# Kernel tuning notes

Hardware: AMD Instinct MI355X
Metric: run time of the kernel (lower is better)

## Reference

```python
import jax, jax.numpy as jnp
import numpy as np

N = 10000      # nodes
E = 160000     # edges (before self-loops)
H = 8          # heads
D_IN, D_H1, D_H2 = 165, 128, 1    # per-head channels of gat1 / gat2
HID = H * D_H1                    # 1024


def batchnorm(x, gamma, beta, eps=1e-5):
    # training-mode BatchNorm1d: biased batch statistics over the node axis
    mu = x.mean(0)
    var = x.var(0)
    return (x - mu) * jax.lax.rsqrt(var + eps) * gamma + beta


def gatv2(x, src, dst, Wl, bl, Wr, br, att, bias, heads, out_ch, concat, n_nodes):
    # PyG GATv2Conv: lin_l on source, lin_r on target; e = att . LeakyReLU(xl_j + xr_i)
    xl = (x @ Wl + bl).reshape(n_nodes, heads, out_ch)   # source transform
    xr = (x @ Wr + br).reshape(n_nodes, heads, out_ch)   # target transform
    e = jax.nn.leaky_relu(xl[src] + xr[dst], 0.2)        # [E,H,C]
    logits = jnp.einsum('ehc,hc->eh', e, att)            # [E,H]
    # segment softmax over incoming edges of each destination node
    m = jax.lax.stop_gradient(jax.ops.segment_max(logits, dst, num_segments=n_nodes))
    a = jnp.exp(logits - m[dst])
    s = jax.ops.segment_sum(a, dst, num_segments=n_nodes)
    alpha = a / (s[dst] + 1e-16)                          # [E,H]
    out = jax.ops.segment_sum(xl[src] * alpha[..., None], dst, num_segments=n_nodes)
    out = out.reshape(n_nodes, heads * out_ch) if concat else out.mean(1)
    return out + bias


def setup_inputs() -> dict:
    key = jax.random.key(0)
    ks = jax.random.split(key, 12)
    g = lambda k, shape, fan_in: jax.random.normal(k, shape, jnp.float32) * (1.0 / np.sqrt(fan_in))
    return {
        'x': jax.random.normal(ks[0], (N, D_IN), jnp.float32),
        'gamma1': jnp.ones((D_IN,), jnp.float32),
        'beta1': jnp.zeros((D_IN,), jnp.float32),
        'Wl1': g(ks[1], (D_IN, HID), D_IN),
        'bl1': jnp.zeros((HID,), jnp.float32),
        'Wr1': g(ks[2], (D_IN, HID), D_IN),
        'br1': jnp.zeros((HID,), jnp.float32),
        'att1': g(ks[3], (H, D_H1), D_H1),
        'bias1': jnp.zeros((HID,), jnp.float32),
        'gamma2': jnp.ones((HID,), jnp.float32),
        'beta2': jnp.zeros((HID,), jnp.float32),
        'Wl2': g(ks[4], (HID, H * D_H2), HID),
        'bl2': jnp.zeros((H * D_H2,), jnp.float32),
        'Wr2': g(ks[5], (HID, H * D_H2), HID),
        'br2': jnp.zeros((H * D_H2,), jnp.float32),
        'att2': g(ks[6], (H, D_H2), D_H2),
        'bias2': jnp.zeros((D_H2,), jnp.float32),
        'edge_index': jax.random.randint(ks[7], (2, E), 0, N, jnp.int64 if jax.config.jax_enable_x64 else jnp.int32),
    }


def reference(x, gamma1, beta1, Wl1, bl1, Wr1, br1, att1, bias1,
              gamma2, beta2, Wl2, bl2, Wr2, br2, att2, bias2, edge_index):
    loops = jnp.arange(N, dtype=edge_index.dtype)
    src = jnp.concatenate([edge_index[0], loops])   # add_self_loops=True (PyG default)
    dst = jnp.concatenate([edge_index[1], loops])
    h = batchnorm(x, gamma1, beta1)
    h = gatv2(h, src, dst, Wl1, bl1, Wr1, br1, att1, bias1, H, D_H1, True, N)
    h = batchnorm(h, gamma2, beta2)
    h = jax.nn.leaky_relu(h, 0.01)                  # F.leaky_relu default slope
    out = gatv2(h, src, dst, Wl2, bl2, Wr2, br2, att2, bias2, H, D_H2, False, N)
    return out
```

## Files before the change

### kernel.cpp

```cpp
#include <hip/hip_runtime.h>

#define NN   10000
#define E0   160000
#define ET   170000
#define DIN  165
#define KP   192
#define HID  1024
#define NH   8
#define BP   200
#define K2P  1032


typedef __bf16 bf16x8 __attribute__((ext_vector_type(8)));
typedef float  f32x4  __attribute__((ext_vector_type(4)));

__device__ __forceinline__ float bf2f(unsigned short u) {
    unsigned int i = ((unsigned int)u) << 16;
    return __builtin_bit_cast(float, i);
}
__device__ __forceinline__ unsigned short f2bf(float f) {
    unsigned int i = __builtin_bit_cast(unsigned int, f);
    i += 0x7fffu + ((i >> 16) & 1u);
    return (unsigned short)(i >> 16);
}
__device__ __forceinline__ float fin(float x) {
    return fminf(fmaxf(x, -1e30f), 1e30f);
}
__device__ __forceinline__ int clampi(int s) {
    return min(max(s, 0), NN - 1);
}
__device__ __forceinline__ void unpack8(uint4 u, float* f) {
    f[0]=bf2f((unsigned short)(u.x)); f[1]=bf2f((unsigned short)(u.x>>16));
    f[2]=bf2f((unsigned short)(u.y)); f[3]=bf2f((unsigned short)(u.y>>16));
    f[4]=bf2f((unsigned short)(u.z)); f[5]=bf2f((unsigned short)(u.z>>16));
    f[6]=bf2f((unsigned short)(u.w)); f[7]=bf2f((unsigned short)(u.w>>16));
}

__global__ __launch_bounds__(256) void debug_fill(float* __restrict__ out, float val) {
    int i = blockIdx.x * 256 + threadIdx.x;
    if (i < NN) out[i] = val;
}

__global__ __launch_bounds__(256) void bn1_stats(const float* __restrict__ x,
                                                 float* __restrict__ colsum, float* __restrict__ colsq) {
    int r0 = blockIdx.x * 125;
    int c = threadIdx.x;
    if (c >= DIN) return;
    float acc = 0.f, sq = 0.f;
    for (int r = r0; r < r0 + 125; ++r) {
        float v = x[(size_t)r * DIN + c];
        acc += v; sq += v * v;
    }
    atomicAdd(&colsum[c], acc);
    atomicAdd(&colsq[c], sq);
}

__global__ __launch_bounds__(256) void bn1_apply(const float* __restrict__ x,
                                                 const float* __restrict__ colsum, const float* __restrict__ colsq,
                                                 const float* __restrict__ gamma, const float* __restrict__ beta,
                                                 unsigned short* __restrict__ hn) {
    int idx = blockIdx.x * 256 + threadIdx.x;
    if (idx >= NN * KP) return;
    int r = idx / KP, c = idx - r * KP;
    float v = 0.f;
    if (c < DIN) {
        float mu  = colsum[c] * (1.f / NN);
        float var = fmaxf(colsq[c] * (1.f / NN) - mu * mu, 0.f);
        float a = gamma[c] * rsqrtf(var + 1e-5f);
        float b = beta[c] - mu * a;
        v = fin(x[(size_t)r * DIN + c] * a + b);
    }
    hn[idx] = f2bf(v);
}

__global__ __launch_bounds__(256) void w1_transpose(const float* __restrict__ wl,
                                                    const float* __restrict__ wr,
                                                    unsigned short* __restrict__ wlt,
                                                    unsigned short* __restrict__ wrt) {
    const float* src    = blockIdx.z ? wr  : wl;
    unsigned short* dst = blockIdx.z ? wrt : wlt;
    __shared__ float ts[32][65];
    const int k0 = blockIdx.x * 32;
    const int n0 = blockIdx.y * 64;
    const int tid = threadIdx.x;
    for (int idx = tid; idx < 32 * 64; idx += 256) {
        int k = idx >> 6, n = idx & 63;
        ts[k][n] = (k0 + k < DIN) ? src[(size_t)(k0 + k) * HID + n0 + n] : 0.f;
    }
    __syncthreads();
    for (int idx = tid; idx < 64 * 32; idx += 256) {
        int n = idx >> 5, k = idx & 31;
        dst[(size_t)(n0 + n) * KP + k0 + k] = f2bf(ts[k][n]);
    }
}

__global__ __launch_bounds__(256) void gemm1_kernel(
    const unsigned short* __restrict__ hn,
    const unsigned short* __restrict__ wlt,
    const unsigned short* __restrict__ wrt,
    const float* __restrict__ bl,
    const float* __restrict__ br,
    unsigned short* __restrict__ xl,
    unsigned short* __restrict__ xr) {
    const unsigned short* wt = blockIdx.z ? wrt : wlt;
    const float* bias        = blockIdx.z ? br  : bl;
    unsigned short* xout     = blockIdx.z ? xr  : xl;

    __shared__ unsigned short bs[64 * BP];
    const int tid  = threadIdx.x;
    const int lane = tid & 63;
    const int wave = tid >> 6;
    const int col  = lane & 15;
    const int q    = lane >> 4;
    const int n0   = blockIdx.y * 64;

    for (int idx = tid; idx < 64 * 48; idx += 256) {
        int r = idx / 48, c = idx - r * 48;
        uint2 v = *(const uint2*)(wt + (size_t)(n0 + r) * KP + c * 4);
        *(uint2*)&bs[r * BP + c * 4] = v;
    }
    __syncthreads();

    const int mbase = blockIdx.x * 128 + wave * 32;
    const int am0 = mbase + col;
    const int am1 = am0 + 16;
    const bool aok0 = (am0 < NN), aok1 = (am1 < NN);

    f32x4 acc[2][4];
    #pragma unroll
    for (int m = 0; m < 2; ++m)
        for (int nt = 0; nt < 4; ++nt)
            for (int r = 0; r < 4; ++r) acc[m][nt][r] = 0.f;

    #pragma unroll
    for (int kt = 0; kt < 6; ++kt) {
        const int kk = kt * 32 + q * 8;
        uint4 a0u = make_uint4(0u,0u,0u,0u), a1u = make_uint4(0u,0u,0u,0u);
        if (aok0) a0u = *(const uint4*)(hn + (size_t)am0 * KP + kk);
        if (aok1) a1u = *(const uint4*)(hn + (size_t)am1 * KP + kk);
        bf16x8 a0 = __builtin_bit_cast(bf16x8, a0u);
        bf16x8 a1 = __builtin_bit_cast(bf16x8, a1u);
        #pragma unroll
        for (int nt = 0; nt < 4; ++nt) {
            bf16x8 bf = __builtin_bit_cast(bf16x8, *(const uint4*)&bs[(nt * 16 + col) * BP + kk]);
            acc[0][nt] = __builtin_amdgcn_mfma_f32_16x16x32_bf16(a0, bf, acc[0][nt], 0, 0, 0);
            acc[1][nt] = __builtin_amdgcn_mfma_f32_16x16x32_bf16(a1, bf, acc[1][nt], 0, 0, 0);
        }
    }

    #pragma unroll
    for (int nt = 0; nt < 4; ++nt) {
        const int nc = n0 + nt * 16 + col;
        const float bv = bias[nc];
        #pragma unroll
        for (int m = 0; m < 2; ++m) {
            #pragma unroll
            for (int r = 0; r < 4; ++r) {
                const int row = mbase + m * 16 + q * 4 + r;
                if (row < NN)
                    xout[(size_t)row * HID + nc] = f2bf(fin(acc[m][nt][r] + bv));
            }
        }
    }
}

__global__ __launch_bounds__(256) void edge_hist(const int* __restrict__ ei, int* __restrict__ deg) {
    int e = blockIdx.x * 256 + threadIdx.x;
    if (e >= ET) return;
    int d = (e < E0) ? ei[E0 + e] : (e - E0);
    atomicAdd(&deg[clampi(d)], 1);
}

__global__ __launch_bounds__(1024) void scan_kernel(const int* __restrict__ deg,
                                                    int* __restrict__ offs, int* __restrict__ cur) {
    __shared__ int wsum[16];
    const int tid = threadIdx.x;
    const int base = tid * 10;
    int loc[10];
    int run = 0;
    #pragma unroll
    for (int j = 0; j < 10; ++j) {
        int idx = base + j;
        int v = (idx < NN) ? deg[idx] : 0;
        loc[j] = run;
        run += v;
    }
    const int lane = tid & 63;
    const int w = tid >> 6;
    int inc = run;
    #pragma unroll
    for (int s = 1; s < 64; s <<= 1) {
        int t = __shfl_up(inc, s);
        if (lane >= s) inc += t;
    }
    if (lane == 63) wsum[w] = inc;
    __syncthreads();
    int woff = 0;
    #pragma unroll
    for (int k = 0; k < 16; ++k) woff += (k < w) ? wsum[k] : 0;
    const int toff = woff + inc - run;
    #pragma unroll
    for (int j = 0; j < 10; ++j) {
        int idx = base + j;
        if (idx < NN) { int e = toff + loc[j]; offs[idx] = e; cur[idx] = e; }
    }
    if (tid == 1023) offs[NN] = woff + inc;
}

__global__ __launch_bounds__(256) void edge_scatter(const int* __restrict__ ei,
                                                    int* __restrict__ cur, int* __restrict__ ssrc) {
    int e = blockIdx.x * 256 + threadIdx.x;
    if (e >= ET) return;
    int s, d;
    if (e < E0) { s = ei[e]; d = ei[E0 + e]; }
    else        { s = e - E0; d = e - E0; }
    int pos = atomicAdd(&cur[clampi(d)], 1);
    if (pos >= 0 && pos < ET) ssrc[pos] = clampi(s);
}

__global__ __launch_bounds__(256) void gat1_node(
    const unsigned short* __restrict__ xl1, const unsigned short* xr1,
    const float* __restrict__ att1, const float* __restrict__ bias1,
    const int* __restrict__ offs, const int* __restrict__ ssrc,
    unsigned short* agg) {
    const int lane = threadIdx.x & 63;
    const int wave = threadIdx.x >> 6;
    const int i = blockIdx.x * 4 + wave;
    const int e0 = offs[i];
    const int e1 = max(offs[i + 1], e0);

    float xr_r[16], att_r[16];
    {
        const uint4* xp = (const uint4*)(xr1 + (size_t)i * HID + lane * 16);
        uint4 u0 = xp[0], u1 = xp[1];
        unpack8(u0, xr_r); unpack8(u1, xr_r + 8);
        const float4* ap = (const float4*)(att1 + lane * 16);
        float4 a0 = ap[0], a1 = ap[1], a2 = ap[2], a3 = ap[3];
        att_r[0]=a0.x; att_r[1]=a0.y; att_r[2]=a0.z; att_r[3]=a0.w;
        att_r[4]=a1.x; att_r[5]=a1.y; att_r[6]=a1.z; att_r[7]=a1.w;
        att_r[8]=a2.x; att_r[9]=a2.y; att_r[10]=a2.z; att_r[11]=a2.w;
        att_r[12]=a3.x; att_r[13]=a3.y; att_r[14]=a3.z; att_r[15]=a3.w;
    }

    float o[16];
    #pragma unroll
    for (int j = 0; j < 16; ++j) o[j] = 0.f;
    float s = 0.f;

    int e = e0;
    for (; e + 1 < e1; e += 2) {
        const int s0i = clampi(ssrc[e]);
        const int s1i = clampi(ssrc[e + 1]);
        const uint4* xp0 = (const uint4*)(xl1 + (size_t)s0i * HID + lane * 16);
        const uint4* xp1 = (const uint4*)(xl1 + (size_t)s1i * HID + lane * 16);
        uint4 a0 = xp0[0], a1 = xp0[1], b0 = xp1[0], b1 = xp1[1];
        float xv0[16], xv1[16];
        unpack8(a0, xv0); unpack8(a1, xv0 + 8);
        unpack8(b0, xv1); unpack8(b1, xv1 + 8);
        float p0 = 0.f, p1 = 0.f;
        #pragma unroll
        for (int j = 0; j < 16; ++j) {
            float v0 = xv0[j] + xr_r[j];
            float v1 = xv1[j] + xr_r[j];
            v0 = fmaxf(v0, 0.2f * v0);
            v1 = fmaxf(v1, 0.2f * v1);
            p0 = fmaf(att_r[j], v0, p0);
            p1 = fmaf(att_r[j], v1, p1);
        }
        p0 += __shfl_xor(p0, 1); p0 += __shfl_xor(p0, 2); p0 += __shfl_xor(p0, 4);
        p1 += __shfl_xor(p1, 1); p1 += __shfl_xor(p1, 2); p1 += __shfl_xor(p1, 4);
        const float aa0 = __expf(fminf(fin(p0), 50.f));
        const float aa1 = __expf(fminf(fin(p1), 50.f));
        s += aa0 + aa1;
        #pragma unroll
        for (int j = 0; j < 16; ++j) o[j] = fmaf(aa0, xv0[j], fmaf(aa1, xv1[j], o[j]));
    }
    if (e < e1) {
        const int sidx = clampi(ssrc[e]);
        const uint4* xp = (const uint4*)(xl1 + (size_t)sidx * HID + lane * 16);
        uint4 u0 = xp[0], u1 = xp[1];
        float xv[16];
        unpack8(u0, xv); unpack8(u1, xv + 8);
        float p = 0.f;
        #pragma unroll
        for (int j = 0; j < 16; ++j) {
            float v = xv[j] + xr_r[j];
            v = fmaxf(v, 0.2f * v);
            p = fmaf(att_r[j], v, p);
        }
        p += __shfl_xor(p, 1); p += __shfl_xor(p, 2); p += __shfl_xor(p, 4);
        const float a = __expf(fminf(fin(p), 50.f));
        s += a;
        #pragma unroll
        for (int j = 0; j < 16; ++j) o[j] = fmaf(a, xv[j], o[j]);
    }

    const float inv = 1.f / (s + 1e-16f);
    const float4* bp = (const float4*)(bias1 + lane * 16);
    float4 b0 = bp[0], b1 = bp[1], b2 = bp[2], b3 = bp[3];
    float bb[16] = {b0.x,b0.y,b0.z,b0.w, b1.x,b1.y,b1.z,b1.w,
                    b2.x,b2.y,b2.z,b2.w, b3.x,b3.y,b3.z,b3.w};
    unsigned short ov[16];
    #pragma unroll
    for (int j = 0; j < 16; ++j) ov[j] = f2bf(fin(o[j] * inv + bb[j]));
    uint4* op = (uint4*)(agg + (size_t)i * HID + lane * 16);
    op[0] = *(const uint4*)&ov[0];
    op[1] = *(const uint4*)&ov[8];
}

__global__ __launch_bounds__(256) void bn2_stats(const unsigned short* __restrict__ agg,
                                                 float* __restrict__ colsum, float* __restrict__ colsq) {
    int r0 = blockIdx.x * 125;
    int t = threadIdx.x;
    float s0=0,s1=0,s2=0,s3=0,q0=0,q1=0,q2=0,q3=0;
    for (int r = r0; r < r0 + 125; ++r) {
        const ushort4 u = *(const ushort4*)(agg + (size_t)r * HID + t * 4);
        float v0=bf2f(u.x), v1=bf2f(u.y), v2=bf2f(u.z), v3=bf2f(u.w);
        s0+=v0; q0+=v0*v0; s1+=v1; q1+=v1*v1;
        s2+=v2; q2+=v2*v2; s3+=v3; q3+=v3*v3;
    }
    atomicAdd(&colsum[t*4+0], s0); atomicAdd(&colsq[t*4+0], q0);
    atomicAdd(&colsum[t*4+1], s1); atomicAdd(&colsq[t*4+1], q1);
    atomicAdd(&colsum[t*4+2], s2); atomicAdd(&colsq[t*4+2], q2);
    atomicAdd(&colsum[t*4+3], s3); atomicAdd(&colsq[t*4+3], q3);
}

__global__ __launch_bounds__(256) void bn2_apply(unsigned short* __restrict__ agg,
                                                 const float* __restrict__ colsum, const float* __restrict__ colsq,
                                                 const float* __restrict__ gamma, const float* __restrict__ beta) {
    int idx = blockIdx.x * 256 + threadIdx.x;
    int base = idx * 4;
    int c = base & (HID - 1);
    ushort4 u = *(const ushort4*)(agg + base);
    float4 cs = *(const float4*)(colsum + c);
    float4 cq = *(const float4*)(colsq + c);
    float4 g  = *(const float4*)(gamma + c);
    float4 bt = *(const float4*)(beta + c);
    float mu0 = cs.x*(1.f/NN), mu1 = cs.y*(1.f/NN), mu2 = cs.z*(1.f/NN), mu3 = cs.w*(1.f/NN);
    float a0 = g.x * rsqrtf(fmaxf(cq.x*(1.f/NN)-mu0*mu0, 0.f) + 1e-5f);
    float a1 = g.y * rsqrtf(fmaxf(cq.y*(1.f/NN)-mu1*mu1, 0.f) + 1e-5f);
    float a2 = g.z * rsqrtf(fmaxf(cq.z*(1.f/NN)-mu2*mu2, 0.f) + 1e-5f);
    float a3 = g.w * rsqrtf(fmaxf(cq.w*(1.f/NN)-mu3*mu3, 0.f) + 1e-5f);
    float o0 = bf2f(u.x)*a0 + (bt.x - mu0*a0);
    float o1 = bf2f(u.y)*a1 + (bt.y - mu1*a1);
    float o2 = bf2f(u.z)*a2 + (bt.z - mu2*a2);
    float o3 = bf2f(u.w)*a3 + (bt.w - mu3*a3);
    o0 = fmaxf(o0, 0.01f * o0); o1 = fmaxf(o1, 0.01f * o1);
    o2 = fmaxf(o2, 0.01f * o2); o3 = fmaxf(o3, 0.01f * o3);
    ushort4 o; o.x = f2bf(fin(o0)); o.y = f2bf(fin(o1)); o.z = f2bf(fin(o2)); o.w = f2bf(fin(o3));
    *(ushort4*)(agg + base) = o;
}

__global__ __launch_bounds__(256) void gemm2_kernel(
    const unsigned short* __restrict__ h2,
    const float* __restrict__ wl2, const float* __restrict__ wr2,
    const float* __restrict__ bl2, const float* __restrict__ br2,
    float* __restrict__ xl2, float* __restrict__ xr2) {
    __shared__ unsigned short bs[16 * K2P];
    const int tid  = threadIdx.x;
    const int lane = tid & 63;
    const int wave = tid >> 6;
    const int col  = lane & 15;
    const int q    = lane >> 4;

    for (int idx = tid; idx < 16 * HID; idx += 256) {
        int n = idx >> 10, k = idx & (HID - 1);
        float v = (n < 8) ? wl2[k * 8 + n] : wr2[k * 8 + (n - 8)];
        bs[n * K2P + k] = f2bf(v);
    }
    __syncthreads();

    const int mtile = blockIdx.x * 4 + wave;
    if (mtile >= NN / 16) return;
    const int m0 = mtile * 16;
    const int am = m0 + col;

    f32x4 acc;
    acc[0] = acc[1] = acc[2] = acc[3] = 0.f;
    #pragma unroll
    for (int kt = 0; kt < 32; ++kt) {
        const int kk = kt * 32 + q * 8;
        bf16x8 af = __builtin_bit_cast(bf16x8, *(const uint4*)(h2 + (size_t)am * HID + kk));
        bf16x8 bf = __builtin_bit_cast(bf16x8, *(const uint4*)&bs[col * K2P + kk]);
        acc = __builtin_amdgcn_mfma_f32_16x16x32_bf16(af, bf, acc, 0, 0, 0);
    }

    const float bv = (col < 8) ? bl2[col] : br2[col - 8];
    float* outp = (col < 8) ? (xl2 + col) : (xr2 + (col - 8));
    #pragma unroll
    for (int r = 0; r < 4; ++r) {
        const int row = m0 + q * 4 + r;
        outp[row * 8] = fin(acc[r] + bv);
    }
}

__global__ __launch_bounds__(256) void gat2_node(
    const float* __restrict__ xl2, const float* __restrict__ xr2,
    const float* __restrict__ att2, const float* __restrict__ bias2,
    const int* __restrict__ offs, const int* __restrict__ ssrc,
    float* __restrict__ out) {
    const int lane = threadIdx.x & 63;
    const int wave = threadIdx.x >> 6;
    const int i = blockIdx.x * 4 + wave;
    const int h = lane & 7, slot = lane >> 3;
    const int e0 = offs[i];
    const int e1 = max(offs[i + 1], e0);
    const float xr_h = xr2[i * 8 + h];
    const float att_h = att2[h];
    float ssum = 0.f, wsum = 0.f;
    for (int eb = e0; eb < e1; eb += 8) {
        int e = eb + slot;
        if (e < e1) {
            float xlv = xl2[clampi(ssrc[e]) * 8 + h];
            float v = xlv + xr_h;
            v = fmaxf(v, 0.2f * v);
            float a = __expf(fminf(fin(att_h * v), 50.f));
            ssum += a; wsum += a * xlv;
        }
    }
    ssum += __shfl_xor(ssum, 8); ssum += __shfl_xor(ssum, 16); ssum += __shfl_xor(ssum, 32);
    wsum += __shfl_xor(wsum, 8); wsum += __shfl_xor(wsum, 16); wsum += __shfl_xor(wsum, 32);
    float v = fin(wsum / (ssum + 1e-16f));
    v += __shfl_xor(v, 1); v += __shfl_xor(v, 2); v += __shfl_xor(v, 4);
    if (lane == 0) out[i] = fin(v * 0.125f + bias2[0]);
}

extern "C" void kernel_launch(void* const* d_in, const int* in_sizes, int n_in,
                              void* d_out, int out_size, void* d_ws, size_t ws_size,
                              hipStream_t stream) {
    float* out = (float*)d_out;

    static const int expected[18] = {
        NN * DIN, DIN, DIN, DIN * HID, HID, DIN * HID, HID, HID, HID,
        HID, HID, HID * NH, NH, HID * NH, NH, NH, 1, 2 * E0
    };
    if (n_in != 18) {
        debug_fill<<<(NN + 255) / 256, 256, 0, stream>>>(out, 8192.f + 64.f * (float)n_in);
        return;
    }
    for (int i = 0; i < 18; ++i) {
        if (in_sizes[i] != expected[i]) {
            debug_fill<<<(NN + 255) / 256, 256, 0, stream>>>(out, 4096.f + 32.f * (float)i);
            return;
        }
    }

    const float* x      = (const float*)d_in[0];
    const float* gamma1 = (const float*)d_in[1];
    const float* beta1  = (const float*)d_in[2];
    const float* Wl1    = (const float*)d_in[3];
    const float* bl1    = (const float*)d_in[4];
    const float* Wr1    = (const float*)d_in[5];
    const float* br1    = (const float*)d_in[6];
    const float* att1   = (const float*)d_in[7];
    const float* bias1  = (const float*)d_in[8];
    const float* gamma2 = (const float*)d_in[9];
    const float* beta2  = (const float*)d_in[10];
    const float* Wl2    = (const float*)d_in[11];
    const float* bl2    = (const float*)d_in[12];
    const float* Wr2    = (const float*)d_in[13];
    const float* br2    = (const float*)d_in[14];
    const float* att2   = (const float*)d_in[15];
    const float* bias2  = (const float*)d_in[16];
    const int*   ei     = (const int*)d_in[17];

    char* p = (char*)d_ws;
    auto alloc = [&](size_t bytes) -> void* {
        void* r = (void*)p;
        p += (bytes + 255) & ~(size_t)255;
        return r;
    };
    unsigned short* xl1  = (unsigned short*)alloc((size_t)NN * HID * 2);
    unsigned short* xr1  = (unsigned short*)alloc((size_t)NN * HID * 2);
    unsigned short* agg  = xr1;
    unsigned short* hn   = (unsigned short*)alloc((size_t)NN * KP * 2);
    unsigned short* wlt  = (unsigned short*)alloc((size_t)HID * KP * 2);
    unsigned short* wrt  = (unsigned short*)alloc((size_t)HID * KP * 2);
    float*          xl2  = (float*)alloc((size_t)NN * 8 * 4);
    float*          xr2  = (float*)alloc((size_t)NN * 8 * 4);
    int*            offs = (int*)alloc((NN + 1) * 4);
    int*            cur  = (int*)alloc(NN * 4);
    int*            ssrc = (int*)alloc(ET * 4);
    char* zbase = p;
    float* colsum1 = (float*)alloc(DIN * 4);
    float* colsq1  = (float*)alloc(DIN * 4);
    float* colsum2 = (float*)alloc(HID * 4);
    float* colsq2  = (float*)alloc(HID * 4);
    int*   deg     = (int*)alloc(NN * 4);
    size_t zlen = (size_t)(p - zbase);
    hipMemsetAsync(zbase, 0, zlen, stream);

    bn1_stats<<<80, 256, 0, stream>>>(x, colsum1, colsq1);
    bn1_apply<<<(NN * KP + 255) / 256, 256, 0, stream>>>(x, colsum1, colsq1, gamma1, beta1, hn);
    w1_transpose<<<dim3(6, 16, 2), 256, 0, stream>>>(Wl1, Wr1, wlt, wrt);
    gemm1_kernel<<<dim3((NN + 127) / 128, HID / 64, 2), 256, 0, stream>>>(hn, wlt, wrt, bl1, br1, xl1, xr1);
    edge_hist<<<(ET + 255) / 256, 256, 0, stream>>>(ei, deg);
    scan_kernel<<<1, 1024, 0, stream>>>(deg, offs, cur);
    edge_scatter<<<(ET + 255) / 256, 256, 0, stream>>>(ei, cur, ssrc);
    gat1_node<<<NN / 4, 256, 0, stream>>>(xl1, xr1, att1, bias1, offs, ssrc, agg);
    bn2_stats<<<80, 256, 0, stream>>>(agg, colsum2, colsq2);
    bn2_apply<<<(NN * HID / 4 + 255) / 256, 256, 0, stream>>>(agg, colsum2, colsq2, gamma2, beta2);
    gemm2_kernel<<<(NN / 16 + 3) / 4, 256, 0, stream>>>(agg, Wl2, Wr2, bl2, br2, xl2, xr2);
    gat2_node<<<NN / 4, 256, 0, stream>>>(xl2, xr2, att2, bias2, offs, ssrc, out);
}
```

Baseline: 288.0 us.

## Fuse BN2 apply into gemm2 and schedule node kernels by descending degree

BatchNorm2 normalisation and LeakyReLU move into the gemm2 A-operand load. Per-column scale and shift are computed into shared memory, which removes the bn2_apply pass that read and wrote the 20MB hidden activation. Separately, the scan kernel now builds a degree-sorted node permutation through a 64-bin counting sort. gat1_node and gat2_node process nodes in descending-degree order to reduce load imbalance across waves. The costs are extra ALU work inside the gemm2 inner loop and a perm indirection, which breaks sequential output locality.

```diff
diff --git a/kernel.cpp b/kernel.cpp
--- a/kernel.cpp
+++ b/kernel.cpp
@@ -172,8 +172,11 @@
 }
 
 __global__ __launch_bounds__(1024) void scan_kernel(const int* __restrict__ deg,
-                                                    int* __restrict__ offs, int* __restrict__ cur) {
+                                                    int* __restrict__ offs, int* __restrict__ cur,
+                                                    int* __restrict__ perm) {
     __shared__ int wsum[16];
+    __shared__ int bins[64];
+    __shared__ int bcur[64];
     const int tid = threadIdx.x;
     const int base = tid * 10;
     int loc[10];
@@ -194,6 +197,7 @@
         if (lane >= s) inc += t;
     }
     if (lane == 63) wsum[w] = inc;
+    if (tid < 64) bins[tid] = 0;
     __syncthreads();
     int woff = 0;
     #pragma unroll
@@ -202,9 +206,32 @@
     #pragma unroll
     for (int j = 0; j < 10; ++j) {
         int idx = base + j;
-        if (idx < NN) { int e = toff + loc[j]; offs[idx] = e; cur[idx] = e; }
+        if (idx < NN) {
+            int e = toff + loc[j]; offs[idx] = e; cur[idx] = e;
+            atomicAdd(&bins[63 - min(deg[idx], 63)], 1);
+        }
     }
     if (tid == 1023) offs[NN] = woff + inc;
+    __syncthreads();
+    if (tid < 64) {
+        int v = bins[tid];
+        int binc = v;
+        #pragma unroll
+        for (int s = 1; s < 64; s <<= 1) {
+            int t = __shfl_up(binc, s);
+            if (tid >= s) binc += t;
+        }
+        bcur[tid] = binc - v;
+    }
+    __syncthreads();
+    #pragma unroll
+    for (int j = 0; j < 10; ++j) {
+        int idx = base + j;
+        if (idx < NN) {
+            int pos = atomicAdd(&bcur[63 - min(deg[idx], 63)], 1);
+            perm[pos] = idx;
+        }
+    }
 }
 
 __global__ __launch_bounds__(256) void edge_scatter(const int* __restrict__ ei,
@@ -222,10 +249,11 @@
     const unsigned short* __restrict__ xl1, const unsigned short* xr1,
     const float* __restrict__ att1, const float* __restrict__ bias1,
     const int* __restrict__ offs, const int* __restrict__ ssrc,
+    const int* __restrict__ perm,
     unsigned short* agg) {
     const int lane = threadIdx.x & 63;
     const int wave = threadIdx.x >> 6;
-    const int i = blockIdx.x * 4 + wave;
+    const int i = perm[blockIdx.x * 4 + wave];
     const int e0 = offs[i];
     const int e1 = max(offs[i + 1], e0);
 
@@ -325,38 +353,15 @@
     atomicAdd(&colsum[t*4+3], s3); atomicAdd(&colsq[t*4+3], q3);
 }
 
-__global__ __launch_bounds__(256) void bn2_apply(unsigned short* __restrict__ agg,
-                                                 const float* __restrict__ colsum, const float* __restrict__ colsq,
-                                                 const float* __restrict__ gamma, const float* __restrict__ beta) {
-    int idx = blockIdx.x * 256 + threadIdx.x;
-    int base = idx * 4;
-    int c = base & (HID - 1);
-    ushort4 u = *(const ushort4*)(agg + base);
-    float4 cs = *(const float4*)(colsum + c);
-    float4 cq = *(const float4*)(colsq + c);
-    float4 g  = *(const float4*)(gamma + c);
-    float4 bt = *(const float4*)(beta + c);
-    float mu0 = cs.x*(1.f/NN), mu1 = cs.y*(1.f/NN), mu2 = cs.z*(1.f/NN), mu3 = cs.w*(1.f/NN);
-    float a0 = g.x * rsqrtf(fmaxf(cq.x*(1.f/NN)-mu0*mu0, 0.f) + 1e-5f);
-    float a1 = g.y * rsqrtf(fmaxf(cq.y*(1.f/NN)-mu1*mu1, 0.f) + 1e-5f);
-    float a2 = g.z * rsqrtf(fmaxf(cq.z*(1.f/NN)-mu2*mu2, 0.f) + 1e-5f);
-    float a3 = g.w * rsqrtf(fmaxf(cq.w*(1.f/NN)-mu3*mu3, 0.f) + 1e-5f);
-    float o0 = bf2f(u.x)*a0 + (bt.x - mu0*a0);
-    float o1 = bf2f(u.y)*a1 + (bt.y - mu1*a1);
-    float o2 = bf2f(u.z)*a2 + (bt.z - mu2*a2);
-    float o3 = bf2f(u.w)*a3 + (bt.w - mu3*a3);
-    o0 = fmaxf(o0, 0.01f * o0); o1 = fmaxf(o1, 0.01f * o1);
-    o2 = fmaxf(o2, 0.01f * o2); o3 = fmaxf(o3, 0.01f * o3);
-    ushort4 o; o.x = f2bf(fin(o0)); o.y = f2bf(fin(o1)); o.z = f2bf(fin(o2)); o.w = f2bf(fin(o3));
-    *(ushort4*)(agg + base) = o;
-}
-
 __global__ __launch_bounds__(256) void gemm2_kernel(
-    const unsigned short* __restrict__ h2,
+    const unsigned short* __restrict__ agg,
+    const float* __restrict__ colsum, const float* __restrict__ colsq,
+    const float* __restrict__ gamma, const float* __restrict__ beta,
     const float* __restrict__ wl2, const float* __restrict__ wr2,
     const float* __restrict__ bl2, const float* __restrict__ br2,
     float* __restrict__ xl2, float* __restrict__ xr2) {
     __shared__ unsigned short bs[16 * K2P];
+    __shared__ float a2s[HID], b2s[HID];
     const int tid  = threadIdx.x;
     const int lane = tid & 63;
     const int wave = tid >> 6;
@@ -368,6 +373,12 @@
         float v = (n < 8) ? wl2[k * 8 + n] : wr2[k * 8 + (n - 8)];
         bs[n * K2P + k] = f2bf(v);
     }
+    for (int c = tid; c < HID; c += 256) {
+        float mu  = colsum[c] * (1.f / NN);
+        float var = fmaxf(colsq[c] * (1.f / NN) - mu * mu, 0.f);
+        float a = gamma[c] * rsqrtf(var + 1e-5f);
+        a2s[c] = a; b2s[c] = beta[c] - mu * a;
+    }
     __syncthreads();
 
     const int mtile = blockIdx.x * 4 + wave;
@@ -380,7 +391,17 @@
     #pragma unroll
     for (int kt = 0; kt < 32; ++kt) {
         const int kk = kt * 32 + q * 8;
-        bf16x8 af = __builtin_bit_cast(bf16x8, *(const uint4*)(h2 + (size_t)am * HID + kk));
+        uint4 u = *(const uint4*)(agg + (size_t)am * HID + kk);
+        float xv[8];
+        unpack8(u, xv);
+        unsigned short hv[8];
+        #pragma unroll
+        for (int j = 0; j < 8; ++j) {
+            float v = xv[j] * a2s[kk + j] + b2s[kk + j];
+            v = fmaxf(v, 0.01f * v);
+            hv[j] = f2bf(fin(v));
+        }
+        bf16x8 af = __builtin_bit_cast(bf16x8, *(const uint4*)hv);
         bf16x8 bf = __builtin_bit_cast(bf16x8, *(const uint4*)&bs[col * K2P + kk]);
         acc = __builtin_amdgcn_mfma_f32_16x16x32_bf16(af, bf, acc, 0, 0, 0);
     }
@@ -398,10 +419,11 @@
     const float* __restrict__ xl2, const float* __restrict__ xr2,
     const float* __restrict__ att2, const float* __restrict__ bias2,
     const int* __restrict__ offs, const int* __restrict__ ssrc,
+    const int* __restrict__ perm,
     float* __restrict__ out) {
     const int lane = threadIdx.x & 63;
     const int wave = threadIdx.x >> 6;
-    const int i = blockIdx.x * 4 + wave;
+    const int i = perm[blockIdx.x * 4 + wave];
     const int h = lane & 7, slot = lane >> 3;
     const int e0 = offs[i];
     const int e1 = max(offs[i + 1], e0);
@@ -481,6 +503,7 @@
     int*            offs = (int*)alloc((NN + 1) * 4);
     int*            cur  = (int*)alloc(NN * 4);
     int*            ssrc = (int*)alloc(ET * 4);
+    int*            perm = (int*)alloc(NN * 4);
     char* zbase = p;
     float* colsum1 = (float*)alloc(DIN * 4);
     float* colsq1  = (float*)alloc(DIN * 4);
@@ -495,11 +518,11 @@
     w1_transpose<<<dim3(6, 16, 2), 256, 0, stream>>>(Wl1, Wr1, wlt, wrt);
     gemm1_kernel<<<dim3((NN + 127) / 128, HID / 64, 2), 256, 0, stream>>>(hn, wlt, wrt, bl1, br1, xl1, xr1);
     edge_hist<<<(ET + 255) / 256, 256, 0, stream>>>(ei, deg);
-    scan_kernel<<<1, 1024, 0, stream>>>(deg, offs, cur);
+    scan_kernel<<<1, 1024, 0, stream>>>(deg, offs, cur, perm);
     edge_scatter<<<(ET + 255) / 256, 256, 0, stream>>>(ei, cur, ssrc);
-    gat1_node<<<NN / 4, 256, 0, stream>>>(xl1, xr1, att1, bias1, offs, ssrc, agg);
+    gat1_node<<<NN / 4, 256, 0, stream>>>(xl1, xr1, att1, bias1, offs, ssrc, perm, agg);
     bn2_stats<<<80, 256, 0, stream>>>(agg, colsum2, colsq2);
-    bn2_apply<<<(NN * HID / 4 + 255) / 256, 256, 0, stream>>>(agg, colsum2, colsq2, gamma2, beta2);
-    gemm2_kernel<<<(NN / 16 + 3) / 4, 256, 0, stream>>>(agg, Wl2, Wr2, bl2, br2, xl2, xr2);
-    gat2_node<<<NN / 4, 256, 0, stream>>>(xl2, xr2, att2, bias2, offs, ssrc, out);
-}
+    gemm2_kernel<<<(NN / 16 + 3) / 4, 256, 0, stream>>>(agg, colsum2, colsq2, gamma2, beta2,
+                                                        Wl2, Wr2, bl2, br2, xl2, xr2);
+    gat2_node<<<NN / 4, 256, 0, stream>>>(xl2, xr2, att2, bias2, offs, ssrc, perm, out);
+}
```

After: 282.7 us. Within noise of the previous version (-1.8%).
